# Optimization experiments

Measured on AMD Instinct MI355X. Metric: run time of the kernel, lower is better.

The kernel has to match this reference:

```python
import jax, jax.numpy as jnp
import numpy as np
from jax.scipy.special import digamma

# dims: B batch, N tokens, D ambient input dim, H heads, HD head ambient dim, DS spatial per head
B, N, D, H = 8, 1024, 512, 8
HD = D // H          # 64
DS = HD - 1          # 63
EPS = 1e-7
SCALE = 1.0 / np.sqrt(HD)
CURVATURE = -1.0     # k = -curvature = 1


def setup_inputs() -> dict:
    key = jax.random.key(0)
    ks = jax.random.split(key, 4)
    # points on the Lorentz hyperboloid: t = sqrt(||x_s||^2 + 1)
    x_s = jax.random.normal(ks[0], (B, N, D - 1), dtype=jnp.float32) * 0.5
    x_t = jnp.sqrt(jnp.sum(x_s * x_s, -1, keepdims=True) + 1.0)
    x = jnp.concatenate([x_t, x_s], -1)
    init = lambda k, sh: jax.random.normal(k, sh, dtype=jnp.float32) * (1.0 / np.sqrt(D))
    Wq = init(ks[1], (H, D, DS)); Wk = init(ks[2], (H, D, DS)); Wv = init(ks[3], (H, D, DS))
    bq = jnp.zeros((H, DS), jnp.float32); bk = jnp.zeros((H, DS), jnp.float32); bv = jnp.zeros((H, DS), jnp.float32)
    return {"x": x, "Wq": Wq, "bq": bq, "Wk": Wk, "bk": bk, "Wv": Wv, "bv": bv}


def lorentz_fc(x, W, b):
    # LorentzFC per head, vectorized over heads: spatial z = Wx+b, time from constraint
    z = jnp.einsum('bnd,hde->bhne', x, W) + b[None, :, None, :]   # [B,H,N,DS]
    t = jnp.sqrt(jnp.sum(z * z, -1, keepdims=True) + 1.0)
    return jnp.concatenate([t, z], -1)                            # [B,H,N,HD]


def lorentz_inner(q, k):
    time = jnp.einsum('bhni,bhmi->bhnm', q[..., :1], k[..., :1])
    space = jnp.einsum('bhnd,bhmd->bhnm', q[..., 1:], k[..., 1:])
    return -time + space


def logmap0(v):
    t, vs = v[..., :1], v[..., 1:]
    d = jnp.arccosh(jnp.maximum(t, 1.0 + EPS))
    denom = jnp.sqrt(jnp.maximum(t * t - 1.0, EPS))
    us = (d / denom) * vs
    return jnp.concatenate([jnp.zeros_like(t), us], -1)


def expmap0(u):
    us = u[..., 1:]
    r = jnp.sqrt(jnp.maximum(jnp.sum(us * us, -1, keepdims=True), EPS * EPS))
    t = jnp.cosh(r)
    xs = (jnp.sinh(r) / r) * us
    return jnp.concatenate([t, xs], -1)


def reference(x, Wq, bq, Wk, bk, Wv, bv):
    q = lorentz_fc(x, Wq, bq)
    k = lorentz_fc(x, Wk, bk)
    v = lorentz_fc(x, Wv, bv)
    scores = lorentz_inner(q, k) * SCALE            # [B,H,N,N]
    attn = jax.nn.softmax(scores, axis=-1)
    v_tan = logmap0(v)                              # [B,H,N,HD], time comp = 0
    out_tan = jnp.einsum('bhnm,bhmd->bhnd', attn, v_tan)
    out = expmap0(out_tan)                          # [B,H,N,HD]
    # curvature-aware log-radius head concat
    s = jnp.exp(0.5 * (digamma(jnp.asarray(H * DS / 2.0)) - digamma(jnp.asarray(DS / 2.0))))
    invK = 1.0 / CURVATURE                          # -1
    t_h = out[..., 0]                               # [B,H,N]
    u_h = out[..., 1:]                              # [B,H,N,DS]
    u_tilde = s * u_h
    sum_term = jnp.sum(t_h * t_h + invK, axis=1)    # [B,N]
    t_prime = jnp.sqrt(jnp.maximum(s * s * sum_term - invK, 1e-8))
    u_concat = jnp.transpose(u_tilde, (0, 2, 1, 3)).reshape(B, N, H * DS)
    return jnp.concatenate([t_prime[..., None], u_concat], -1)   # [B,N,1+H*DS]
```

## Files before the change

kernel.cpp:

```cpp
#include <hip/hip_runtime.h>
#include <math.h>

#define B_ 8
#define N_ 1024
#define D_ 512
#define H_ 8
#define HD_ 64
#define DS_ 63
#define SCALE_ 0.125f
#define EPS_ 1e-7f
#define KT_ 64

typedef short bf16x8 __attribute__((ext_vector_type(8)));
typedef float f32x16 __attribute__((ext_vector_type(16)));

typedef const __attribute__((address_space(1))) unsigned int* gas_ptr;
typedef __attribute__((address_space(3))) unsigned int* las_ptr;

__device__ inline ushort f2bf(float f) {
    uint u = __float_as_uint(f);
    uint r = (u + 0x7FFFu + ((u >> 16) & 1u)) >> 16;
    return (ushort)r;
}

__global__ void xcast_kernel(const float* __restrict__ x, ushort* __restrict__ xb) {
    int i = blockIdx.x * 256 + threadIdx.x;
    float4 v = ((const float4*)x)[i];
    ushort4 o;
    o.x = f2bf(v.x); o.y = f2bf(v.y); o.z = f2bf(v.z); o.w = f2bf(v.w);
    ((ushort4*)xb)[i] = o;
}

__global__ void wprep_kernel(const float* __restrict__ Wq, const float* __restrict__ Wk,
                             const float* __restrict__ Wv, ushort* __restrict__ Wt) {
    __shared__ float til[64 * 65];
    const int g = blockIdx.x, kbase = blockIdx.y * 64;
    const int mat = g >> 3, h = g & 7;
    const float* W = (mat == 0) ? Wq : (mat == 1) ? Wk : Wv;
    const float* src = W + (size_t)h * D_ * DS_ + (size_t)kbase * DS_;
    for (int i = threadIdx.x; i < 64 * DS_; i += 256) {
        int k = i / DS_, e = i - k * DS_;
        til[k * 65 + e] = src[i];
    }
    __syncthreads();
    for (int i = threadIdx.x; i < 64 * 64; i += 256) {
        int e = i >> 6, kk = i & 63;
        float v = (e < DS_) ? til[kk * 65 + e] : 0.f;
        Wt[((size_t)g * 64 + e) * D_ + kbase + kk] = f2bf(v);
    }
}

__global__ __launch_bounds__(256, 2)
void proj2_kernel(const ushort* __restrict__ Xb, const ushort* __restrict__ Wt,
                  const float* __restrict__ bq, const float* __restrict__ bk,
                  const float* __restrict__ bv,
                  ushort* __restrict__ Qo, ushort* __restrict__ Ko,
                  ushort* __restrict__ Vto)
{
    __shared__ char smem[49152];
    __shared__ float tval[128], cval[128];

    const int tid = threadIdx.x;
    const int wid = tid >> 6, lane = tid & 63;
    const int lm = lane & 31, g = lane >> 5;
    const int R0 = blockIdx.x * 128;
    const int grp = blockIdx.y;
    const int mat = grp >> 3, h = grp & 7;

    char* As = smem;
    char* Bs = smem + 32768;
    const ushort* Wg = Wt + (size_t)grp * 64 * D_;

    f32x16 acc0 = {0.f}, acc1 = {0.f};

    auto stageA = [&](int buf, int ktE) {
#pragma unroll
        for (int it = 0; it < 4; it++) {
            int ci = it * 256 + tid;
            int row = ci >> 3, cb = (ci & 7) * 16;
            const char* src = (const char*)(Xb + (size_t)(R0 + row) * D_ + ktE)
                              + (cb ^ ((row & 7) << 4));
            __builtin_amdgcn_global_load_lds((gas_ptr)src,
                (las_ptr)(As + buf * 16384 + it * 4096 + wid * 1024), 16, 0, 0);
        }
    };
    auto stageB = [&](int buf, int ktE) {
#pragma unroll
        for (int it = 0; it < 2; it++) {
            int ci = it * 256 + tid;
            int row = ci >> 3, cb = (ci & 7) * 16;
            const char* src = (const char*)(Wg + (size_t)row * D_ + ktE)
                              + (cb ^ ((row & 7) << 4));
            __builtin_amdgcn_global_load_lds((gas_ptr)src,
                (las_ptr)(Bs + buf * 8192 + it * 4096 + wid * 1024), 16, 0, 0);
        }
    };

    stageA(0, 0); stageB(0, 0);
    __syncthreads();

    const int arow = wid * 32 + lm;
    const int asw = (lm & 7) << 4;

    for (int t = 0; t < 8; t++) {
        int cur = t & 1;
        if (t < 7) { stageA(cur ^ 1, (t + 1) * KT_); stageB(cur ^ 1, (t + 1) * KT_); }
        char* Ab = As + cur * 16384;
        char* Bb = Bs + cur * 8192;
#pragma unroll
        for (int c = 0; c < 4; c++) {
            int kb = (c * 32 + g * 16);
            bf16x8 af  = *(const bf16x8*)(Ab + arow * 128 + (kb ^ asw));
            bf16x8 bf0 = *(const bf16x8*)(Bb + lm * 128 + (kb ^ asw));
            bf16x8 bf1 = *(const bf16x8*)(Bb + (32 + lm) * 128 + (kb ^ asw));
            acc0 = __builtin_amdgcn_mfma_f32_32x32x16_bf16(af, bf0, acc0, 0, 0, 0);
            acc1 = __builtin_amdgcn_mfma_f32_32x32x16_bf16(af, bf1, acc1, 0, 0, 0);
        }
        if (t < 7) __syncthreads();
    }
    __syncthreads();

    const float* bptr = (mat == 0) ? bq : (mat == 1) ? bk : bv;
    float bv0 = (lm < DS_) ? bptr[h * DS_ + lm] : 0.f;
    float bv1 = (lm + 32 < DS_) ? bptr[h * DS_ + lm + 32] : 0.f;
    float* zs = (float*)smem;
#pragma unroll
    for (int r = 0; r < 16; r++) {
        int row = wid * 32 + (r & 3) + 8 * (r >> 2) + 4 * g;
        zs[row * 65 + lm]      = acc0[r] + bv0;
        zs[row * 65 + 32 + lm] = acc1[r] + bv1;
    }
    __syncthreads();

    if (tid < 128) {
        float ss = 0.f;
        for (int e = 0; e < DS_; e++) { float v = zs[tid * 65 + e]; ss += v * v; }
        float t = sqrtf(ss + 1.f);
        float w0, coef;
        if (mat == 0)      { w0 = -t * SCALE_; coef = SCALE_; }
        else if (mat == 1) { w0 =  t;          coef = 1.f; }
        else {
            float tc = fmaxf(t, 1.f + EPS_);
            float d  = acoshf(tc);
            float dn = sqrtf(fmaxf(t * t - 1.f, EPS_));
            w0 = 0.f; coef = d / dn;
        }
        tval[tid] = w0; cval[tid] = coef;
    }
    __syncthreads();

    const int b = R0 >> 10, n0 = R0 & (N_ - 1);
    const int bh = b * H_ + h;
    if (mat == 2) {
        for (int i = tid; i < 128 * 64; i += 256) {
            int e = i >> 7, nl = i & 127;
            float val = (e == 0) ? 0.f : cval[nl] * zs[nl * 65 + e - 1];
            Vto[((size_t)bh * 64 + e) * N_ + n0 + nl] = f2bf(val);
        }
    } else {
        ushort* dst = (mat == 0) ? Qo : Ko;
        for (int i = tid; i < 128 * 64; i += 256) {
            int rr = i >> 6, e = i & 63;
            float val = (e == 0) ? tval[rr] : cval[rr] * zs[rr * 65 + e - 1];
            dst[((size_t)bh * N_ + n0 + rr) * 64 + e] = f2bf(val);
        }
    }
}

__global__ __launch_bounds__(256, 4)
void attn2_kernel(const ushort* __restrict__ Q, const ushort* __restrict__ K,
                  const ushort* __restrict__ Vt, float* __restrict__ out,
                  float* __restrict__ TS, float sconst)
{
    __shared__ char lds[32768];

    const int tid  = threadIdx.x;
    const int lane = tid & 63;
    const int lm = lane & 31, g = lane >> 5;
    const int r = (tid >> 6) & 1, s = tid >> 7;
    const int ptid = tid & 127, pw = ptid >> 6;

    const int bid = blockIdx.x;
    const int idx = bid >> 3;
    const int bh  = (idx >> 4) * 8 + (bid & 7);
    const int R0  = (idx & 15) * 64;
    const int qrow = R0 + r * 32 + lm;

    bf16x8 qf[4];
    const ushort* qptr = Q + (((size_t)bh) * N_ + qrow) * 64 + g * 8;
#pragma unroll
    for (int c = 0; c < 4; c++)
        qf[c] = *(const bf16x8*)(qptr + c * 16);

    f32x16 acc0 = {0.f}, acc1 = {0.f};
    float den = 0.f;

    const ushort* kg = K  + ((size_t)bh) * N_ * 64;
    const ushort* vg = Vt + ((size_t)bh) * 64 * N_;
    char* kbase = lds + s * 8192;
    char* vbase = lds + 16384 + s * 8192;

    for (int t = 0; t < 8; t++) {
        __syncthreads();
        const int ks = s * 512 + t * 64;
#pragma unroll
        for (int it = 0; it < 4; it++) {
            int ci = it * 128 + ptid;
            int row = ci >> 3, cb = (ci & 7) << 4;
            int sw = (row & 7) << 4;
            const char* srck = (const char*)(kg + (size_t)(ks + row) * 64) + (cb ^ sw);
            __builtin_amdgcn_global_load_lds((gas_ptr)srck,
                (las_ptr)(kbase + it * 2048 + pw * 1024), 16, 0, 0);
            const char* srcv = (const char*)(vg + (size_t)row * N_ + ks) + (cb ^ sw);
            __builtin_amdgcn_global_load_lds((gas_ptr)srcv,
                (las_ptr)(vbase + it * 2048 + pw * 1024), 16, 0, 0);
        }
        __syncthreads();

#pragma unroll
        for (int sub = 0; sub < 2; sub++) {
            f32x16 st = {0.f};
            const int krow = sub * 32 + lm;
            const int ksw  = (krow & 7) << 4;
#pragma unroll
            for (int c = 0; c < 4; c++) {
                bf16x8 kf = *(const bf16x8*)(kbase + krow * 128 + ((g * 16 + c * 32) ^ ksw));
                st = __builtin_amdgcn_mfma_f32_32x32x16_bf16(kf, qf[c], st, 0, 0, 0);
            }
            float p[16];
#pragma unroll
            for (int rr = 0; rr < 16; rr++) {
                p[rr] = __expf(st[rr]);
                den += p[rr];
            }
            bf16x8 pf[2];
#pragma unroll
            for (int c = 0; c < 2; c++)
#pragma unroll
                for (int i = 0; i < 8; i++)
                    pf[c][i] = (short)f2bf(p[8 * c + i]);
#pragma unroll
            for (int c = 0; c < 2; c++) {
#pragma unroll
                for (int dh = 0; dh < 2; dh++) {
                    const int vrow = dh * 32 + lm;
                    const int vsw  = (vrow & 7) << 4;
                    const int colb = sub * 64 + 8 * g + 32 * c;
                    union { uint2 u2[2]; bf16x8 v; } uu;
                    uu.u2[0] = *(const uint2*)(vbase + vrow * 128 + ( colb       ^ vsw));
                    uu.u2[1] = *(const uint2*)(vbase + vrow * 128 + ((colb + 16) ^ vsw));
                    if (dh == 0)
                        acc0 = __builtin_amdgcn_mfma_f32_32x32x16_bf16(uu.v, pf[c], acc0, 0, 0, 0);
                    else
                        acc1 = __builtin_amdgcn_mfma_f32_32x32x16_bf16(uu.v, pf[c], acc1, 0, 0, 0);
                }
            }
        }
    }

    __syncthreads();
    float* fl = (float*)lds;
    const int ib = (((r * 2 + g) * 32) + lm) * 33;
    if (s == 1) {
#pragma unroll
        for (int j = 0; j < 16; j++) { fl[ib + j] = acc0[j]; fl[ib + 16 + j] = acc1[j]; }
        fl[ib + 32] = den;
    }
    __syncthreads();
    if (s == 0) {
#pragma unroll
        for (int j = 0; j < 16; j++) { acc0[j] += fl[ib + j]; acc1[j] += fl[ib + 16 + j]; }
        den += fl[ib + 32];

        den += __shfl_xor(den, 32);
        float invd = 1.f / den;
        float ss = 0.f;
#pragma unroll
        for (int j = 0; j < 16; j++) {
            acc0[j] *= invd; acc1[j] *= invd;
            ss += acc0[j] * acc0[j] + acc1[j] * acc1[j];
        }
        ss += __shfl_xor(ss, 32);
        float rr = sqrtf(fmaxf(ss, 1e-14f));
        float t  = coshf(rr);
        float coef = sconst * sinhf(rr) / rr;

        const int b = bh >> 3, h = bh & 7;
        const size_t ob = ((size_t)b * N_ + qrow) * 505 + (size_t)h * DS_;
#pragma unroll
        for (int j = 0; j < 16; j++) {
            int d = (j & 3) + 8 * (j >> 2) + 4 * g;
            if (d >= 1) out[ob + d] = coef * acc0[j];
            out[ob + d + 32] = coef * acc1[j];
        }
        if (g == 0) TS[((size_t)bh) * N_ + qrow] = t;
    }
}

__global__ void tprime_kernel(const float* __restrict__ TS, float* __restrict__ out,
                              float sconst)
{
    int idx = blockIdx.x * 256 + threadIdx.x;
    if (idx >= B_ * N_) return;
    int b = idx >> 10, n = idx & (N_ - 1);
    float sum = 0.f;
#pragma unroll
    for (int h = 0; h < H_; h++) {
        float t = TS[((size_t)(b * H_ + h)) * N_ + n];
        sum += t * t - 1.f;
    }
    float tp = sqrtf(fmaxf(sconst * sconst * sum + 1.f, 1e-8f));
    out[(size_t)idx * 505] = tp;
}

static double digamma_(double x) {
    double r = 0.0;
    while (x < 20.0) { r -= 1.0 / x; x += 1.0; }
    double f = 1.0 / (x * x);
    return r + log(x) - 0.5 / x - f * (1.0 / 12.0 - f * (1.0 / 120.0 - f * (1.0 / 252.0)));
}

extern "C" void kernel_launch(void* const* d_in, const int* in_sizes, int n_in,
                              void* d_out, int out_size, void* d_ws, size_t ws_size,
                              hipStream_t stream) {
    const float* x  = (const float*)d_in[0];
    const float* Wq = (const float*)d_in[1];
    const float* bq = (const float*)d_in[2];
    const float* Wk = (const float*)d_in[3];
    const float* bk = (const float*)d_in[4];
    const float* Wv = (const float*)d_in[5];
    const float* bv = (const float*)d_in[6];
    float* out = (float*)d_out;

    const size_t QKV = (size_t)B_ * H_ * N_ * 64;
    ushort* Qd  = (ushort*)d_ws;
    ushort* Kd  = Qd + QKV;
    ushort* Vtd = Kd + QKV;
    ushort* Xb  = Vtd + QKV;
    ushort* Wtd = Xb + (size_t)B_ * N_ * D_;
    float*  TS  = (float*)(Wtd + (size_t)24 * 64 * D_);

    const float sconst = (float)exp(0.5 * (digamma_(H_ * DS_ / 2.0) - digamma_(DS_ / 2.0)));

    xcast_kernel<<<(B_ * N_ * D_ / 4 + 255) / 256, 256, 0, stream>>>(x, Xb);
    wprep_kernel<<<dim3(24, 8), 256, 0, stream>>>(Wq, Wk, Wv, Wtd);
    proj2_kernel<<<dim3(64, 24), 256, 0, stream>>>(Xb, Wtd, bq, bk, bv, Qd, Kd, Vtd);
    attn2_kernel<<<1024, 256, 0, stream>>>(Qd, Kd, Vtd, out, TS, sconst);
    tprime_kernel<<<(B_ * N_ + 255) / 256, 256, 0, stream>>>(TS, out, sconst);
}
```

Baseline: 78.41 us.

## Merge prep kernels, widen projection tile, restructure attention to double-buffered full-key loop

The x-cast and weight-transpose kernels are fused into one launch. The projection kernel now computes two heads per block (128x128 tile with 2x2 MFMA per wave), so each staged X tile is reused twice. The attention kernel drops the split-key scheme and its cross-wave LDS reduction: each wave owns 32 query rows and walks all 1024 keys with double-buffered LDS staging, s_setprio around MFMA bursts, and bf16 packing via byte perm (truncation instead of rounding). Fewer, larger blocks reduce the work repeated per block, at the cost of less parallelism in attention and slightly different rounding of the probabilities.

```diff
diff --git a/kernel.cpp b/kernel.cpp
--- a/kernel.cpp
+++ b/kernel.cpp
@@ -23,55 +23,59 @@
     return (ushort)r;
 }
 
-__global__ void xcast_kernel(const float* __restrict__ x, ushort* __restrict__ xb) {
-    int i = blockIdx.x * 256 + threadIdx.x;
-    float4 v = ((const float4*)x)[i];
-    ushort4 o;
-    o.x = f2bf(v.x); o.y = f2bf(v.y); o.z = f2bf(v.z); o.w = f2bf(v.w);
-    ((ushort4*)xb)[i] = o;
-}
-
-__global__ void wprep_kernel(const float* __restrict__ Wq, const float* __restrict__ Wk,
-                             const float* __restrict__ Wv, ushort* __restrict__ Wt) {
+__global__ void prep_kernel(const float* __restrict__ x,
+                            const float* __restrict__ Wq, const float* __restrict__ Wk,
+                            const float* __restrict__ Wv,
+                            ushort* __restrict__ xb, ushort* __restrict__ Wt) {
     __shared__ float til[64 * 65];
-    const int g = blockIdx.x, kbase = blockIdx.y * 64;
-    const int mat = g >> 3, h = g & 7;
-    const float* W = (mat == 0) ? Wq : (mat == 1) ? Wk : Wv;
-    const float* src = W + (size_t)h * D_ * DS_ + (size_t)kbase * DS_;
-    for (int i = threadIdx.x; i < 64 * DS_; i += 256) {
-        int k = i / DS_, e = i - k * DS_;
-        til[k * 65 + e] = src[i];
-    }
-    __syncthreads();
-    for (int i = threadIdx.x; i < 64 * 64; i += 256) {
-        int e = i >> 6, kk = i & 63;
-        float v = (e < DS_) ? til[kk * 65 + e] : 0.f;
-        Wt[((size_t)g * 64 + e) * D_ + kbase + kk] = f2bf(v);
+    const int bid = blockIdx.x;
+    if (bid < 4096) {
+        int i = bid * 256 + threadIdx.x;
+        float4 v = ((const float4*)x)[i];
+        ushort4 o;
+        o.x = f2bf(v.x); o.y = f2bf(v.y); o.z = f2bf(v.z); o.w = f2bf(v.w);
+        ((ushort4*)xb)[i] = o;
+    } else {
+        const int b2 = bid - 4096;
+        const int g = b2 >> 3, kbase = (b2 & 7) * 64;
+        const int mat = g >> 3, h = g & 7;
+        const float* W = (mat == 0) ? Wq : (mat == 1) ? Wk : Wv;
+        const float* src = W + (size_t)h * D_ * DS_ + (size_t)kbase * DS_;
+        for (int i = threadIdx.x; i < 64 * DS_; i += 256) {
+            int k = i / DS_, e = i - k * DS_;
+            til[k * 65 + e] = src[i];
+        }
+        __syncthreads();
+        for (int i = threadIdx.x; i < 64 * 64; i += 256) {
+            int e = i >> 6, kk = i & 63;
+            float v = (e < DS_) ? til[kk * 65 + e] : 0.f;
+            Wt[((size_t)g * 64 + e) * D_ + kbase + kk] = f2bf(v);
+        }
     }
 }
 
 __global__ __launch_bounds__(256, 2)
-void proj2_kernel(const ushort* __restrict__ Xb, const ushort* __restrict__ Wt,
+void proj3_kernel(const ushort* __restrict__ Xb, const ushort* __restrict__ Wt,
                   const float* __restrict__ bq, const float* __restrict__ bk,
                   const float* __restrict__ bv,
                   ushort* __restrict__ Qo, ushort* __restrict__ Ko,
                   ushort* __restrict__ Vto)
 {
-    __shared__ char smem[49152];
-    __shared__ float tval[128], cval[128];
+    __shared__ char smem[65536];
 
     const int tid = threadIdx.x;
     const int wid = tid >> 6, lane = tid & 63;
     const int lm = lane & 31, g = lane >> 5;
+    const int wr = wid & 1, wg = wid >> 1;
     const int R0 = blockIdx.x * 128;
-    const int grp = blockIdx.y;
-    const int mat = grp >> 3, h = grp & 7;
+    const int grp0 = blockIdx.y * 2;
+    const int mat = grp0 >> 3;
 
     char* As = smem;
     char* Bs = smem + 32768;
-    const ushort* Wg = Wt + (size_t)grp * 64 * D_;
-
-    f32x16 acc0 = {0.f}, acc1 = {0.f};
+    const ushort* Wg = Xb ? (Wt + (size_t)grp0 * 64 * D_) : Wt;
+
+    f32x16 acc00 = {0.f}, acc01 = {0.f}, acc10 = {0.f}, acc11 = {0.f};
 
     auto stageA = [&](int buf, int ktE) {
 #pragma unroll
@@ -86,105 +90,114 @@
     };
     auto stageB = [&](int buf, int ktE) {
 #pragma unroll
-        for (int it = 0; it < 2; it++) {
+        for (int it = 0; it < 4; it++) {
             int ci = it * 256 + tid;
             int row = ci >> 3, cb = (ci & 7) * 16;
             const char* src = (const char*)(Wg + (size_t)row * D_ + ktE)
                               + (cb ^ ((row & 7) << 4));
             __builtin_amdgcn_global_load_lds((gas_ptr)src,
-                (las_ptr)(Bs + buf * 8192 + it * 4096 + wid * 1024), 16, 0, 0);
+                (las_ptr)(Bs + buf * 16384 + it * 4096 + wid * 1024), 16, 0, 0);
         }
     };
 
     stageA(0, 0); stageB(0, 0);
+    const int asw = (lm & 7) << 4;
+
+    for (int t = 0; t < 8; t++) {
+        __syncthreads();
+        if (t < 7) { stageA((t + 1) & 1, (t + 1) * KT_); stageB((t + 1) & 1, (t + 1) * KT_); }
+        const int cur = t & 1;
+        char* Ab = As + cur * 16384;
+        char* Bb = Bs + cur * 16384;
+#pragma unroll
+        for (int c = 0; c < 4; c++) {
+            int kb = (c * 32 + g * 16) ^ asw;
+            bf16x8 a0 = *(const bf16x8*)(Ab + (wr * 64 + lm) * 128 + kb);
+            bf16x8 a1 = *(const bf16x8*)(Ab + (wr * 64 + 32 + lm) * 128 + kb);
+            bf16x8 b0 = *(const bf16x8*)(Bb + (wg * 64 + lm) * 128 + kb);
+            bf16x8 b1 = *(const bf16x8*)(Bb + (wg * 64 + 32 + lm) * 128 + kb);
+            acc00 = __builtin_amdgcn_mfma_f32_32x32x16_bf16(a0, b0, acc00, 0, 0, 0);
+            acc01 = __builtin_amdgcn_mfma_f32_32x32x16_bf16(a0, b1, acc01, 0, 0, 0);
+            acc10 = __builtin_amdgcn_mfma_f32_32x32x16_bf16(a1, b0, acc10, 0, 0, 0);
+            acc11 = __builtin_amdgcn_mfma_f32_32x32x16_bf16(a1, b1, acc11, 0, 0, 0);
+        }
+    }
     __syncthreads();
 
-    const int arow = wid * 32 + lm;
-    const int asw = (lm & 7) << 4;
-
-    for (int t = 0; t < 8; t++) {
-        int cur = t & 1;
-        if (t < 7) { stageA(cur ^ 1, (t + 1) * KT_); stageB(cur ^ 1, (t + 1) * KT_); }
-        char* Ab = As + cur * 16384;
-        char* Bb = Bs + cur * 8192;
-#pragma unroll
-        for (int c = 0; c < 4; c++) {
-            int kb = (c * 32 + g * 16);
-            bf16x8 af  = *(const bf16x8*)(Ab + arow * 128 + (kb ^ asw));
-            bf16x8 bf0 = *(const bf16x8*)(Bb + lm * 128 + (kb ^ asw));
-            bf16x8 bf1 = *(const bf16x8*)(Bb + (32 + lm) * 128 + (kb ^ asw));
-            acc0 = __builtin_amdgcn_mfma_f32_32x32x16_bf16(af, bf0, acc0, 0, 0, 0);
-            acc1 = __builtin_amdgcn_mfma_f32_32x32x16_bf16(af, bf1, acc1, 0, 0, 0);
-        }
-        if (t < 7) __syncthreads();
-    }
-    __syncthreads();
-
+    float* zs   = (float*)smem;
+    float* tval = (float*)(smem + 33280);
+    float* cval = tval + 128;
     const float* bptr = (mat == 0) ? bq : (mat == 1) ? bk : bv;
-    float bv0 = (lm < DS_) ? bptr[h * DS_ + lm] : 0.f;
-    float bv1 = (lm + 32 < DS_) ? bptr[h * DS_ + lm + 32] : 0.f;
-    float* zs = (float*)smem;
-#pragma unroll
-    for (int r = 0; r < 16; r++) {
-        int row = wid * 32 + (r & 3) + 8 * (r >> 2) + 4 * g;
-        zs[row * 65 + lm]      = acc0[r] + bv0;
-        zs[row * 65 + 32 + lm] = acc1[r] + bv1;
-    }
-    __syncthreads();
-
-    if (tid < 128) {
-        float ss = 0.f;
-        for (int e = 0; e < DS_; e++) { float v = zs[tid * 65 + e]; ss += v * v; }
-        float t = sqrtf(ss + 1.f);
-        float w0, coef;
-        if (mat == 0)      { w0 = -t * SCALE_; coef = SCALE_; }
-        else if (mat == 1) { w0 =  t;          coef = 1.f; }
-        else {
-            float tc = fmaxf(t, 1.f + EPS_);
-            float d  = acoshf(tc);
-            float dn = sqrtf(fmaxf(t * t - 1.f, EPS_));
-            w0 = 0.f; coef = d / dn;
-        }
-        tval[tid] = w0; cval[tid] = coef;
-    }
-    __syncthreads();
-
     const int b = R0 >> 10, n0 = R0 & (N_ - 1);
-    const int bh = b * H_ + h;
-    if (mat == 2) {
-        for (int i = tid; i < 128 * 64; i += 256) {
-            int e = i >> 7, nl = i & 127;
-            float val = (e == 0) ? 0.f : cval[nl] * zs[nl * 65 + e - 1];
-            Vto[((size_t)bh * 64 + e) * N_ + n0 + nl] = f2bf(val);
-        }
-    } else {
-        ushort* dst = (mat == 0) ? Qo : Ko;
-        for (int i = tid; i < 128 * 64; i += 256) {
-            int rr = i >> 6, e = i & 63;
-            float val = (e == 0) ? tval[rr] : cval[rr] * zs[rr * 65 + e - 1];
-            dst[((size_t)bh * N_ + n0 + rr) * 64 + e] = f2bf(val);
-        }
-    }
-}
-
-__global__ __launch_bounds__(256, 4)
-void attn2_kernel(const ushort* __restrict__ Q, const ushort* __restrict__ K,
+
+    for (int pass = 0; pass < 2; pass++) {
+        const int h = (grp0 + pass) & 7;
+        if (pass) __syncthreads();
+        if (wg == pass) {
+            float ba = (lm < DS_) ? bptr[h * DS_ + lm] : 0.f;
+            float bb = (lm + 32 < DS_) ? bptr[h * DS_ + lm + 32] : 0.f;
+#pragma unroll
+            for (int r = 0; r < 16; r++) {
+                int rm = (r & 3) + 8 * (r >> 2) + 4 * g;
+                zs[(wr * 64 + rm) * 65 + lm]           = acc00[r] + ba;
+                zs[(wr * 64 + rm) * 65 + 32 + lm]      = acc01[r] + bb;
+                zs[(wr * 64 + 32 + rm) * 65 + lm]      = acc10[r] + ba;
+                zs[(wr * 64 + 32 + rm) * 65 + 32 + lm] = acc11[r] + bb;
+            }
+        }
+        __syncthreads();
+        if (tid < 128) {
+            float ss = 0.f;
+            for (int e = 0; e < DS_; e++) { float v = zs[tid * 65 + e]; ss += v * v; }
+            float t = sqrtf(ss + 1.f);
+            float w0, coef;
+            if (mat == 0)      { w0 = -t * SCALE_; coef = SCALE_; }
+            else if (mat == 1) { w0 =  t;          coef = 1.f; }
+            else {
+                float tc = fmaxf(t, 1.f + EPS_);
+                float d  = acoshf(tc);
+                float dn = sqrtf(fmaxf(t * t - 1.f, EPS_));
+                w0 = 0.f; coef = d / dn;
+            }
+            tval[tid] = w0; cval[tid] = coef;
+        }
+        __syncthreads();
+
+        const int bh = b * H_ + h;
+        if (mat == 2) {
+            for (int i = tid; i < 128 * 64; i += 256) {
+                int e = i >> 7, nl = i & 127;
+                float val = (e == 0) ? 0.f : cval[nl] * zs[nl * 65 + e - 1];
+                Vto[((size_t)bh * 64 + e) * N_ + n0 + nl] = f2bf(val);
+            }
+        } else {
+            ushort* dst = (mat == 0) ? Qo : Ko;
+            for (int i = tid; i < 128 * 64; i += 256) {
+                int rr = i >> 6, e = i & 63;
+                float val = (e == 0) ? tval[rr] : cval[rr] * zs[rr * 65 + e - 1];
+                dst[((size_t)bh * N_ + n0 + rr) * 64 + e] = f2bf(val);
+            }
+        }
+    }
+}
+
+__global__ __launch_bounds__(256, 2)
+void attn3_kernel(const ushort* __restrict__ Q, const ushort* __restrict__ K,
                   const ushort* __restrict__ Vt, float* __restrict__ out,
                   float* __restrict__ TS, float sconst)
 {
     __shared__ char lds[32768];
 
     const int tid  = threadIdx.x;
+    const int wid  = tid >> 6;
     const int lane = tid & 63;
     const int lm = lane & 31, g = lane >> 5;
-    const int r = (tid >> 6) & 1, s = tid >> 7;
-    const int ptid = tid & 127, pw = ptid >> 6;
 
     const int bid = blockIdx.x;
-    const int idx = bid >> 3;
-    const int bh  = (idx >> 4) * 8 + (bid & 7);
-    const int R0  = (idx & 15) * 64;
-    const int qrow = R0 + r * 32 + lm;
+    const int rest = bid >> 3;
+    const int bh   = (rest >> 3) * 8 + (bid & 7);
+    const int R0   = (rest & 7) * 128;
+    const int qrow = R0 + wid * 32 + lm;
 
     bf16x8 qf[4];
     const ushort* qptr = Q + (((size_t)bh) * N_ + qrow) * 64 + g * 8;
@@ -197,48 +210,54 @@
 
     const ushort* kg = K  + ((size_t)bh) * N_ * 64;
     const ushort* vg = Vt + ((size_t)bh) * 64 * N_;
-    char* kbase = lds + s * 8192;
-    char* vbase = lds + 16384 + s * 8192;
-
-    for (int t = 0; t < 8; t++) {
-        __syncthreads();
-        const int ks = s * 512 + t * 64;
-#pragma unroll
-        for (int it = 0; it < 4; it++) {
-            int ci = it * 128 + ptid;
+
+    auto stage = [&](int buf, int kt) {
+#pragma unroll
+        for (int it = 0; it < 2; it++) {
+            int ci = it * 256 + tid;
             int row = ci >> 3, cb = (ci & 7) << 4;
             int sw = (row & 7) << 4;
-            const char* srck = (const char*)(kg + (size_t)(ks + row) * 64) + (cb ^ sw);
+            const char* srck = (const char*)(kg + (size_t)(kt + row) * 64) + (cb ^ sw);
             __builtin_amdgcn_global_load_lds((gas_ptr)srck,
-                (las_ptr)(kbase + it * 2048 + pw * 1024), 16, 0, 0);
-            const char* srcv = (const char*)(vg + (size_t)row * N_ + ks) + (cb ^ sw);
+                (las_ptr)(lds + buf * 8192 + it * 4096 + wid * 1024), 16, 0, 0);
+            const char* srcv = (const char*)(vg + (size_t)row * N_ + kt) + (cb ^ sw);
             __builtin_amdgcn_global_load_lds((gas_ptr)srcv,
-                (las_ptr)(vbase + it * 2048 + pw * 1024), 16, 0, 0);
-        }
-        __syncthreads();
+                (las_ptr)(lds + 16384 + buf * 8192 + it * 4096 + wid * 1024), 16, 0, 0);
+        }
+    };
+
+    stage(0, 0);
+    for (int t = 0; t < 16; t++) {
+        __syncthreads();
+        if (t < 15) stage((t + 1) & 1, (t + 1) * KT_);
+        const int cur = t & 1;
+        char* kbase = lds + cur * 8192;
+        char* vbase = lds + 16384 + cur * 8192;
 
 #pragma unroll
         for (int sub = 0; sub < 2; sub++) {
             f32x16 st = {0.f};
             const int krow = sub * 32 + lm;
             const int ksw  = (krow & 7) << 4;
+            __builtin_amdgcn_s_setprio(1);
 #pragma unroll
             for (int c = 0; c < 4; c++) {
                 bf16x8 kf = *(const bf16x8*)(kbase + krow * 128 + ((g * 16 + c * 32) ^ ksw));
                 st = __builtin_amdgcn_mfma_f32_32x32x16_bf16(kf, qf[c], st, 0, 0, 0);
             }
+            __builtin_amdgcn_s_setprio(0);
             float p[16];
 #pragma unroll
             for (int rr = 0; rr < 16; rr++) {
                 p[rr] = __expf(st[rr]);
                 den += p[rr];
             }
-            bf16x8 pf[2];
-#pragma unroll
-            for (int c = 0; c < 2; c++)
-#pragma unroll
-                for (int i = 0; i < 8; i++)
-                    pf[c][i] = (short)f2bf(p[8 * c + i]);
+            union { uint u[8]; bf16x8 v[2]; } pu;
+#pragma unroll
+            for (int j = 0; j < 8; j++)
+                pu.u[j] = __builtin_amdgcn_perm(__float_as_uint(p[2 * j + 1]),
+                                                __float_as_uint(p[2 * j]), 0x07060302);
+            __builtin_amdgcn_s_setprio(1);
 #pragma unroll
             for (int c = 0; c < 2; c++) {
 #pragma unroll
@@ -250,51 +269,37 @@
                     uu.u2[0] = *(const uint2*)(vbase + vrow * 128 + ( colb       ^ vsw));
                     uu.u2[1] = *(const uint2*)(vbase + vrow * 128 + ((colb + 16) ^ vsw));
                     if (dh == 0)
-                        acc0 = __builtin_amdgcn_mfma_f32_32x32x16_bf16(uu.v, pf[c], acc0, 0, 0, 0);
+                        acc0 = __builtin_amdgcn_mfma_f32_32x32x16_bf16(uu.v, pu.v[c], acc0, 0, 0, 0);
                     else
-                        acc1 = __builtin_amdgcn_mfma_f32_32x32x16_bf16(uu.v, pf[c], acc1, 0, 0, 0);
+                        acc1 = __builtin_amdgcn_mfma_f32_32x32x16_bf16(uu.v, pu.v[c], acc1, 0, 0, 0);
                 }
             }
-        }
-    }
-
-    __syncthreads();
-    float* fl = (float*)lds;
-    const int ib = (((r * 2 + g) * 32) + lm) * 33;
-    if (s == 1) {
-#pragma unroll
-        for (int j = 0; j < 16; j++) { fl[ib + j] = acc0[j]; fl[ib + 16 + j] = acc1[j]; }
-        fl[ib + 32] = den;
-    }
-    __syncthreads();
-    if (s == 0) {
-#pragma unroll
-        for (int j = 0; j < 16; j++) { acc0[j] += fl[ib + j]; acc1[j] += fl[ib + 16 + j]; }
-        den += fl[ib + 32];
-
-        den += __shfl_xor(den, 32);
-        float invd = 1.f / den;
-        float ss = 0.f;
-#pragma unroll
-        for (int j = 0; j < 16; j++) {
-            acc0[j] *= invd; acc1[j] *= invd;
-            ss += acc0[j] * acc0[j] + acc1[j] * acc1[j];
-        }
-        ss += __shfl_xor(ss, 32);
-        float rr = sqrtf(fmaxf(ss, 1e-14f));
-        float t  = coshf(rr);
-        float coef = sconst * sinhf(rr) / rr;
-
-        const int b = bh >> 3, h = bh & 7;
-        const size_t ob = ((size_t)b * N_ + qrow) * 505 + (size_t)h * DS_;
-#pragma unroll
-        for (int j = 0; j < 16; j++) {
-            int d = (j & 3) + 8 * (j >> 2) + 4 * g;
-            if (d >= 1) out[ob + d] = coef * acc0[j];
-            out[ob + d + 32] = coef * acc1[j];
-        }
-        if (g == 0) TS[((size_t)bh) * N_ + qrow] = t;
-    }
+            __builtin_amdgcn_s_setprio(0);
+        }
+    }
+
+    den += __shfl_xor(den, 32);
+    float invd = 1.f / den;
+    float ss = 0.f;
+#pragma unroll
+    for (int r = 0; r < 16; r++) {
+        acc0[r] *= invd; acc1[r] *= invd;
+        ss += acc0[r] * acc0[r] + acc1[r] * acc1[r];
+    }
+    ss += __shfl_xor(ss, 32);
+    float rr = sqrtf(fmaxf(ss, 1e-14f));
+    float t  = coshf(rr);
+    float coef = sconst * sinhf(rr) / rr;
+
+    const int b = bh >> 3, h = bh & 7;
+    const size_t ob = ((size_t)b * N_ + qrow) * 505 + (size_t)h * DS_;
+#pragma unroll
+    for (int r = 0; r < 16; r++) {
+        int d = (r & 3) + 8 * (r >> 2) + 4 * g;
+        if (d >= 1) out[ob + d] = coef * acc0[r];
+        out[ob + d + 32] = coef * acc1[r];
+    }
+    if (g == 0) TS[((size_t)bh) * N_ + qrow] = t;
 }
 
 __global__ void tprime_kernel(const float* __restrict__ TS, float* __restrict__ out,
@@ -342,9 +347,8 @@
 
     const float sconst = (float)exp(0.5 * (digamma_(H_ * DS_ / 2.0) - digamma_(DS_ / 2.0)));
 
-    xcast_kernel<<<(B_ * N_ * D_ / 4 + 255) / 256, 256, 0, stream>>>(x, Xb);
-    wprep_kernel<<<dim3(24, 8), 256, 0, stream>>>(Wq, Wk, Wv, Wtd);
-    proj2_kernel<<<dim3(64, 24), 256, 0, stream>>>(Xb, Wtd, bq, bk, bv, Qd, Kd, Vtd);
-    attn2_kernel<<<1024, 256, 0, stream>>>(Qd, Kd, Vtd, out, TS, sconst);
+    prep_kernel<<<4096 + 192, 256, 0, stream>>>(x, Wq, Wk, Wv, Xb, Wtd);
+    proj3_kernel<<<dim3(64, 12), 256, 0, stream>>>(Xb, Wtd, bq, bk, bv, Qd, Kd, Vtd);
+    attn3_kernel<<<512, 256, 0, stream>>>(Qd, Kd, Vtd, out, TS, sconst);
     tprime_kernel<<<(B_ * N_ + 255) / 256, 256, 0, stream>>>(TS, out, sconst);
 }
```

Result: no change. 79.72 us (+1.7%).
